# Optimization experiments

Measured on AMD Instinct MI355X. Metric: run time of the kernel, lower is better.

## Reference

```python
import jax, jax.numpy as jnp
import numpy as np

B, T, C, V, L, H, HS = 64, 256, 256, 65, 6, 8, 32


def _ln(x, g, b, eps=1e-5):
    mu = jnp.mean(x, axis=-1, keepdims=True)
    var = jnp.mean(jnp.square(x - mu), axis=-1, keepdims=True)
    return (x - mu) * jax.lax.rsqrt(var + eps) * g + b


def setup_inputs() -> dict:
    key = jax.random.key(0)
    ks = jax.random.split(key, 28)
    n = lambda k, s: jax.random.normal(k, s, dtype=jnp.float32) * 0.02
    return {
        "idx": jax.random.randint(ks[0], (B, T), 0, V),
        "targets": jax.random.randint(ks[1], (B, T), 0, V),
        "tok_emb": n(ks[2], (V, C)),
        "pos_emb": n(ks[3], (T, C)),
        "wq": n(ks[4], (L, H, C, HS)), "bq": n(ks[5], (L, H, HS)),
        "wk": n(ks[6], (L, H, C, HS)), "bk": n(ks[7], (L, H, HS)),
        "wv": n(ks[8], (L, H, C, HS)), "bv": n(ks[9], (L, H, HS)),
        "wo": n(ks[10], (L, C, C)), "bo": n(ks[11], (L, C)),
        "ln1_g": jnp.ones((L, C), jnp.float32), "ln1_b": jnp.zeros((L, C), jnp.float32),
        "w1": n(ks[12], (L, C, 4 * C)), "b1": n(ks[13], (L, 4 * C)),
        "w2": n(ks[14], (L, 4 * C, C)), "b2": n(ks[15], (L, C)),
        "ln2_g": jnp.ones((L, C), jnp.float32), "ln2_b": jnp.zeros((L, C), jnp.float32),
        "lnf_g": jnp.ones((C,), jnp.float32), "lnf_b": jnp.zeros((C,), jnp.float32),
        "lm_w": n(ks[16], (C, V)), "lm_b": n(ks[17], (V,)),
    }


def reference(idx, targets, tok_emb, pos_emb, wq, bq, wk, bk, wv, bv, wo, bo,
              ln1_g, ln1_b, w1, b1, w2, b2, ln2_g, ln2_b, lnf_g, lnf_b, lm_w, lm_b):
    Bc, Tc = idx.shape
    x = tok_emb[idx] + pos_emb[:Tc]  # [B,T,C]
    causal = jnp.tril(jnp.ones((Tc, Tc), dtype=bool))
    scale = C ** (-0.5)  # NOTE: original scales by n_embd**-0.5, not head_size
    for l in range(L):
        xn = _ln(x, ln1_g[l], ln1_b[l])
        q = jnp.einsum('btc,hcd->bhtd', xn, wq[l]) + bq[l][None, :, None, :]
        k = jnp.einsum('btc,hcd->bhtd', xn, wk[l]) + bk[l][None, :, None, :]
        v = jnp.einsum('btc,hcd->bhtd', xn, wv[l]) + bv[l][None, :, None, :]
        s = jnp.einsum('bhtd,bhsd->bhts', q, k) * scale
        s = jnp.where(causal, s, -jnp.inf)
        a = jax.nn.softmax(s, axis=-1)  # dropout is identity in eval
        o = jnp.einsum('bhts,bhsd->bhtd', a, v)
        o = o.transpose(0, 2, 1, 3).reshape(Bc, Tc, C)  # concat heads
        x = x + o @ wo[l] + bo[l]
        xn2 = _ln(x, ln2_g[l], ln2_b[l])
        h = jax.nn.relu(xn2 @ w1[l] + b1[l])
        x = x + h @ w2[l] + b2[l]
    x = _ln(x, lnf_g, lnf_b)
    logits = (x @ lm_w + lm_b).reshape(Bc * Tc, V)
    logp = jax.nn.log_softmax(logits, axis=-1)
    tgt = targets.reshape(-1)
    loss = -jnp.mean(logp[jnp.arange(Bc * Tc), tgt])
    return logits, loss
```

## Files before the change

### kernel.cpp

```cpp
#include <hip/hip_runtime.h>
#include <hip/hip_bf16.h>
#include <math.h>

#define BB 64
#define TT 256
#define CC 256
#define VV 65
#define LL 6
#define HH 8
#define BT (BB*TT)

typedef unsigned short u16;
typedef __attribute__((ext_vector_type(8))) _Float16 h8v;
typedef __attribute__((ext_vector_type(4))) float f4v;
typedef __attribute__((ext_vector_type(4))) unsigned short u16x4;

typedef const unsigned int __attribute__((address_space(1))) gu32;
typedef unsigned int       __attribute__((address_space(3))) lu32;

__device__ inline u16 f2h(float f) { _Float16 h = (_Float16)f; return *(u16*)&h; }

__device__ inline void gld_lds16(const void* g, void* l) {
    __builtin_amdgcn_global_load_lds((gu32*)g, (lu32*)l, 16, 0, 0);
}


__device__ inline void pack_dev(const float* __restrict__ src, u16* __restrict__ dst,
                                int K, int N, int NT, int KT, int id) {
    int perLayer = NT * KT * 8192;
    int l = id / perLayer; int rem = id - l * perLayer;
    int tile = rem >> 13, within = rem & 8191;
    int nT = tile / KT, kT = tile - nT * KT;
    int colIn = within >> 6, u = within & 63;
    int s = (u >> 3) ^ (colIn & 7);
    int k = kT * 64 + s * 8 + (u & 7);
    int n = nT * 128 + colIn;
    float v = (n < N) ? src[((size_t)l * K + k) * N + n] : 0.f;
    dst[((size_t)l * NT * KT + tile) * 8192 + within] = f2h(v);
}

#define E_QKV (LL*24*8192)
#define E_WO  (LL*8*8192)
#define E_W1  (LL*32*8192)
#define E_W2  (LL*32*8192)
#define E_LM  (4*8192)
#define E_QB  (LL*768)
#define E_TOT (E_QKV+E_WO+E_W1+E_W2+E_LM+E_QB)

__global__ __launch_bounds__(256)
void pack_all(const float* __restrict__ wq, const float* __restrict__ wk,
              const float* __restrict__ wv, const float* __restrict__ wo,
              const float* __restrict__ w1, const float* __restrict__ w2,
              const float* __restrict__ lmw,
              const float* __restrict__ bq, const float* __restrict__ bk,
              const float* __restrict__ bv,
              u16* __restrict__ qkvT, u16* __restrict__ woT, u16* __restrict__ w1T,
              u16* __restrict__ w2T, u16* __restrict__ lmT, float* __restrict__ Bp) {
    int id = blockIdx.x * 256 + threadIdx.x;
    if (id < E_QKV) {
        const int perLayer = 24 * 8192;
        int l = id / perLayer; int rem = id - l * perLayer;
        int tile = rem >> 13, within = rem & 8191;
        int nT = tile >> 2, kT = tile & 3;
        int colIn = within >> 6, u = within & 63;
        int s = (u >> 3) ^ (colIn & 7);
        int k = kT * 64 + s * 8 + (u & 7);
        int n = nT * 128 + colIn;
        int which = n >> 8, hd = n & 255, h = hd >> 5, d = hd & 31;
        const float* src = (which == 0) ? wq : (which == 1) ? wk : wv;
        float v = src[(((size_t)l * HH + h) * CC + k) * 32 + d];
        qkvT[((size_t)l * 24 + tile) * 8192 + within] = f2h(v);
        return;
    }
    id -= E_QKV;
    if (id < E_WO) { pack_dev(wo, woT, 256, 256, 2, 4, id); return; }
    id -= E_WO;
    if (id < E_W1) { pack_dev(w1, w1T, 256, 1024, 8, 4, id); return; }
    id -= E_W1;
    if (id < E_W2) { pack_dev(w2, w2T, 1024, 256, 2, 16, id); return; }
    id -= E_W2;
    if (id < E_LM) { pack_dev(lmw, lmT, 256, VV, 1, 4, id); return; }
    id -= E_LM;
    if (id < E_QB) {
        int l = id / 768, j = id % 768;
        int which = j >> 8, hd = j & 255, h = hd >> 5, d = hd & 31;
        const float* src = (which == 0) ? bq : (which == 1) ? bk : bv;
        Bp[id] = src[((size_t)l * HH + h) * 32 + d];
    }
}

__global__ __launch_bounds__(256)
void embed_kernel(const int* __restrict__ idx, const float* __restrict__ te,
                  const float* __restrict__ pe, float* __restrict__ x) {
    int i = blockIdx.x * blockDim.x + threadIdx.x;
    if (i >= BT * 64) return;
    int bt = i >> 6, c4 = i & 63;
    int tok = idx[bt];
    int t = bt & (TT - 1);
    float4 a = ((const float4*)te)[(size_t)tok * 64 + c4];
    float4 p = ((const float4*)pe)[(size_t)t * 64 + c4];
    float4 o; o.x = a.x + p.x; o.y = a.y + p.y; o.z = a.z + p.z; o.w = a.w + p.w;
    ((float4*)x)[i] = o;
}

__global__ __launch_bounds__(256)
void ln_kernel(const float* __restrict__ x, const float* __restrict__ g,
               const float* __restrict__ b, u16* __restrict__ outT) {
    int lane = threadIdx.x & 63;
    int wave = threadIdx.x >> 6;
    int row = blockIdx.x * 4 + wave;
    float4 v = ((const float4*)(x + (size_t)row * CC))[lane];
    float s = v.x + v.y + v.z + v.w;
    #pragma unroll
    for (int m = 1; m < 64; m <<= 1) s += __shfl_xor(s, m, 64);
    float mu = s * (1.f / CC);
    float dx = v.x - mu, dy = v.y - mu, dz = v.z - mu, dw = v.w - mu;
    float vs = dx * dx + dy * dy + dz * dz + dw * dw;
    #pragma unroll
    for (int m = 1; m < 64; m <<= 1) vs += __shfl_xor(vs, m, 64);
    float rs = rsqrtf(vs * (1.f / CC) + 1e-5f);
    float4 gv = ((const float4*)g)[lane];
    float4 bv = ((const float4*)b)[lane];
    float o[4];
    o[0] = dx * rs * gv.x + bv.x;
    o[1] = dy * rs * gv.y + bv.y;
    o[2] = dz * rs * gv.z + bv.z;
    o[3] = dw * rs * gv.w + bv.w;
    int rIn = row & 127, mT = row >> 7;
    int kT = lane >> 4;
    int kIn = (lane * 4) & 63;
    int slot = kIn >> 3, j = kIn & 7;
    size_t base = ((size_t)mT * 4 + kT) * 8192;
    int ub = rIn * 64 + ((slot ^ (rIn & 7)) << 3) + j;
    u16x4 hv;
    #pragma unroll
    for (int q = 0; q < 4; ++q) hv[q] = f2h(o[q]);
    *(u16x4*)(outT + base + ub) = hv;
}

template<int EPI>
__global__ __launch_bounds__(512, 4)
void gemm_mfma(const u16* __restrict__ At, const u16* __restrict__ Bt,
               const float* __restrict__ bias, float* __restrict__ Co,
               u16* __restrict__ CoT, int KTfull, int KTc, int NT, int N, int KTout) {
    __shared__ __align__(16) char lds[65536];
    int tid = threadIdx.x;
    int l = tid & 63, w = tid >> 6;
    int nwg = gridDim.x;
    int id = blockIdx.x;
    int cpx = nwg >> 3;
    id = (id & 7) * cpx + (id >> 3);
    int mT = id / NT, nT = id - mT * NT;
    int ktBase = blockIdx.y * KTc;

    const char* Abase = (const char*)(At + ((size_t)mT * KTfull + ktBase) * 8192);
    const char* Bbase = (const char*)(Bt + ((size_t)nT * KTfull + ktBase) * 8192);
    int wm = w >> 1, wn = w & 1;

    f4v acc[2][4];
    #pragma unroll
    for (int i = 0; i < 2; ++i)
        #pragma unroll
        for (int j = 0; j < 4; ++j) acc[i][j] = (f4v)0.f;

    int lrow = l & 15, lg = l >> 4;

    #define STAGE(buf, kt) {                                           \
        char* la = lds + (buf) * 32768 + w * 2048;                     \
        char* lb = lds + (buf) * 32768 + 16384 + w * 2048;             \
        const char* ga = Abase + (kt) * 16384 + w * 2048 + l * 16;     \
        const char* gb = Bbase + (kt) * 16384 + w * 2048 + l * 16;     \
        _Pragma("unroll")                                              \
        for (int j = 0; j < 2; ++j) {                                  \
            gld_lds16(ga + j * 1024, la + j * 1024);                   \
            gld_lds16(gb + j * 1024, lb + j * 1024);                   \
        } }

    STAGE(0, 0);
    __syncthreads();
    int cur = 0;
    for (int kt = 0; kt < KTc; ++kt) {
        if (kt + 1 < KTc) STAGE(cur ^ 1, kt + 1);
        const char* lb0 = lds + cur * 32768;
        #pragma unroll
        for (int kh = 0; kh < 2; ++kh) {
            h8v ah[2], bh[4];
            #pragma unroll
            for (int mi = 0; mi < 2; ++mi) {
                int rc = wm * 32 + mi * 16 + lrow;
                ah[mi] = *(const h8v*)(lb0 + rc * 128 + 16 * ((kh * 4 + lg) ^ (rc & 7)));
            }
            #pragma unroll
            for (int ni = 0; ni < 4; ++ni) {
                int rc = wn * 64 + ni * 16 + lrow;
                bh[ni] = *(const h8v*)(lb0 + 16384 + rc * 128 + 16 * ((kh * 4 + lg) ^ (rc & 7)));
            }
            #pragma unroll
            for (int mi = 0; mi < 2; ++mi)
                #pragma unroll
                for (int ni = 0; ni < 4; ++ni)
                    acc[mi][ni] = __builtin_amdgcn_mfma_f32_16x16x32_f16(ah[mi], bh[ni], acc[mi][ni], 0, 0, 0);
        }
        __syncthreads();
        cur ^= 1;
    }
    #undef STAGE

    int colbase = nT * 128 + wn * 64;
    if (EPI == 0) {
        #pragma unroll
        for (int mi = 0; mi < 2; ++mi) {
            int r0 = mT * 128 + wm * 32 + mi * 16 + lg * 4;
            #pragma unroll
            for (int ni = 0; ni < 4; ++ni) {
                int cg = colbase + ni * 16 + lrow;
                float bv = bias[cg];
                #pragma unroll
                for (int q = 0; q < 4; ++q)
                    CoT[(size_t)(r0 + q) * N + cg] = f2h(acc[mi][ni][q] + bv);
            }
        }
    } else if (EPI == 2) {
        #pragma unroll
        for (int mi = 0; mi < 2; ++mi) {
            int r0 = mT * 128 + wm * 32 + mi * 16 + lg * 4;
            #pragma unroll
            for (int ni = 0; ni < 4; ++ni) {
                int cg = colbase + ni * 16 + lrow;
                float bv = bias[cg];
                int kTo = cg >> 6, kIn = cg & 63;
                size_t tbase = ((size_t)mT * KTout + kTo) * 8192;
                #pragma unroll
                for (int q = 0; q < 4; ++q) {
                    int rIn = (r0 + q) & 127;
                    float f = fmaxf(acc[mi][ni][q] + bv, 0.f);
                    int ub = rIn * 64 + (((kIn >> 3) ^ (rIn & 7)) << 3) + (kIn & 7);
                    CoT[tbase + ub] = f2h(f);
                }
            }
        }
    } else if (EPI == 3) {
        #pragma unroll
        for (int mi = 0; mi < 2; ++mi) {
            int r0 = mT * 128 + wm * 32 + mi * 16 + lg * 4;
            #pragma unroll
            for (int ni = 0; ni < 4; ++ni) {
                int cg = colbase + ni * 16 + lrow;
                if (cg < VV) {
                    float bv = bias[cg];
                    #pragma unroll
                    for (int q = 0; q < 4; ++q)
                        Co[(size_t)(r0 + q) * VV + cg] = acc[mi][ni][q] + bv;
                }
            }
        }
    } else {
        #pragma unroll
        for (int mi = 0; mi < 2; ++mi) {
            int r0 = mT * 128 + wm * 32 + mi * 16 + lg * 4;
            #pragma unroll
            for (int ni = 0; ni < 4; ++ni) {
                int cg = colbase + ni * 16 + lrow;
                float bv = (ktBase == 0) ? bias[cg] : 0.f;
                #pragma unroll
                for (int q = 0; q < 4; ++q)
                    atomicAdd(Co + (size_t)(r0 + q) * N + cg, acc[mi][ni][q] + bv);
            }
        }
    }
}

__global__ __launch_bounds__(256)
void attn_mfma(const u16* __restrict__ qkv, u16* __restrict__ outT) {
    __shared__ __align__(16) char lds[42496];
    int bh = blockIdx.x;
    bh = (bh & 7) * 64 + (bh >> 3);
    int b = bh >> 3, h = bh & 7;
    const u16* base = qkv + (size_t)b * TT * 768;
    int tid = threadIdx.x;
    int w = tid >> 6, l = tid & 63;
    int li = l & 15, g = l >> 4;

    {
        int r0 = tid >> 3, c = tid & 7;
        #pragma unroll
        for (int it = 0; it < 8; ++it) {
            int t = it * 32 + r0;
            u16x4 kv = *(const u16x4*)(base + (size_t)t * 768 + 256 + h * 32 + c * 4);
            u16x4 vv = *(const u16x4*)(base + (size_t)t * 768 + 512 + h * 32 + c * 4);
            *(u16x4*)(lds + t * 80 + c * 8) = kv;
            *(u16*)(lds + 20480 + (c * 4 + 0) * 528 + t * 2) = vv[0];
            *(u16*)(lds + 20480 + (c * 4 + 1) * 528 + t * 2) = vv[1];
            *(u16*)(lds + 20480 + (c * 4 + 2) * 528 + t * 2) = vv[2];
            *(u16*)(lds + 20480 + (c * 4 + 3) * 528 + t * 2) = vv[3];
        }
    }
    __syncthreads();

    char* Pb = lds + 37376 + w * 1280;
    int mts[4] = {w, 7 - w, 8 + w, 15 - w};
    #pragma unroll
    for (int im = 0; im < 4; ++im) {
        int mt = mts[im];
        int mq = mt * 16;
        h8v aq = *(const h8v*)(base + (size_t)(mq + li) * 768 + h * 32 + g * 8);

        f4v o0 = (f4v)0.f, o1 = (f4v)0.f;
        float mrun0 = -1e30f, mrun1 = -1e30f, mrun2 = -1e30f, mrun3 = -1e30f;
        float lrun0 = 0.f, lrun1 = 0.f, lrun2 = 0.f, lrun3 = 0.f;
        int nu = (mt >> 1) + 1;
        for (int kt = 0; kt < nu; ++kt) {
            int kb = kt * 32;
            h8v kf0 = *(const h8v*)(lds + (kb + li) * 80 + g * 16);
            h8v kf1 = *(const h8v*)(lds + (kb + 16 + li) * 80 + g * 16);
            f4v s0 = __builtin_amdgcn_mfma_f32_16x16x32_f16(aq, kf0, (f4v)0.f, 0, 0, 0);
            f4v s1 = __builtin_amdgcn_mfma_f32_16x16x32_f16(aq, kf1, (f4v)0.f, 0, 0, 0);
            bool maskunit = (kt == nu - 1);
            float p0[4], p1[4];
            float* mr[4] = {&mrun0, &mrun1, &mrun2, &mrun3};
            float* lr[4] = {&lrun0, &lrun1, &lrun2, &lrun3};
            #pragma unroll
            for (int qq = 0; qq < 4; ++qq) {
                float v0 = s0[qq] * 0.0625f;
                float v1 = s1[qq] * 0.0625f;
                if (maskunit) {
                    int qg = mq + g * 4 + qq;
                    if (kb + li > qg)      v0 = -1e30f;
                    if (kb + 16 + li > qg) v1 = -1e30f;
                }
                float tm = fmaxf(v0, v1);
                #pragma unroll
                for (int msk = 1; msk < 16; msk <<= 1)
                    tm = fmaxf(tm, __shfl_xor(tm, msk, 64));
                float mold = *mr[qq];
                float mnew = fmaxf(mold, tm);
                float corr = __expf(mold - mnew);
                float e0 = __expf(v0 - mnew);
                float e1 = __expf(v1 - mnew);
                float ts = e0 + e1;
                #pragma unroll
                for (int msk = 1; msk < 16; msk <<= 1)
                    ts += __shfl_xor(ts, msk, 64);
                *lr[qq] = *lr[qq] * corr + ts;
                *mr[qq] = mnew;
                o0[qq] *= corr; o1[qq] *= corr;
                p0[qq] = e0; p1[qq] = e1;
            }
            #pragma unroll
            for (int qq = 0; qq < 4; ++qq) {
                *(u16*)(Pb + (g * 4 + qq) * 80 + li * 2)        = f2h(p0[qq]);
                *(u16*)(Pb + (g * 4 + qq) * 80 + (16 + li) * 2) = f2h(p1[qq]);
            }
            h8v pf  = *(const h8v*)(Pb + li * 80 + g * 16);
            h8v vf0 = *(const h8v*)(lds + 20480 + li * 528        + kb * 2 + g * 16);
            h8v vf1 = *(const h8v*)(lds + 20480 + (16 + li) * 528 + kb * 2 + g * 16);
            o0 = __builtin_amdgcn_mfma_f32_16x16x32_f16(pf, vf0, o0, 0, 0, 0);
            o1 = __builtin_amdgcn_mfma_f32_16x16x32_f16(pf, vf1, o1, 0, 0, 0);
        }
        float invs[4] = {1.f / lrun0, 1.f / lrun1, 1.f / lrun2, 1.f / lrun3};
        #pragma unroll
        for (int qq = 0; qq < 4; ++qq) {
            int tok = mq + g * 4 + qq;
            int rIn = tok & 127;
            size_t tb = ((size_t)(b * 2 + (tok >> 7)) * 4 + (h >> 1)) * 8192;
            float f0 = o0[qq] * invs[qq];
            float f1 = o1[qq] * invs[qq];
            int kIn0 = (h & 1) * 32 + li;
            int kIn1 = kIn0 + 16;
            int ub0 = rIn * 64 + (((kIn0 >> 3) ^ (rIn & 7)) << 3) + (kIn0 & 7);
            int ub1 = rIn * 64 + (((kIn1 >> 3) ^ (rIn & 7)) << 3) + (kIn1 & 7);
            outT[tb + ub0] = f2h(f0);
            outT[tb + ub1] = f2h(f1);
        }
    }
}

__global__ __launch_bounds__(256)
void loss_kernel(const float* __restrict__ lg, const int* __restrict__ tgt,
                 float* __restrict__ loss) {
    int row = blockIdx.x * 256 + threadIdx.x;
    const float* r = lg + (size_t)row * VV;
    float mx = -INFINITY;
    for (int v = 0; v < VV; ++v) mx = fmaxf(mx, r[v]);
    float se = 0.f;
    for (int v = 0; v < VV; ++v) se += __expf(r[v] - mx);
    float nl = mx + __logf(se) - r[tgt[row]];
    #pragma unroll
    for (int m = 1; m < 64; m <<= 1) nl += __shfl_xor(nl, m, 64);
    __shared__ float wsum[4];
    int lane = threadIdx.x & 63, wv = threadIdx.x >> 6;
    if (lane == 0) wsum[wv] = nl;
    __syncthreads();
    if (threadIdx.x == 0)
        atomicAdd(loss, (wsum[0] + wsum[1] + wsum[2] + wsum[3]) * (1.f / BT));
}

extern "C" void kernel_launch(void* const* d_in, const int* in_sizes, int n_in,
                              void* d_out, int out_size, void* d_ws, size_t ws_size,
                              hipStream_t stream) {
    const int*   idx  = (const int*)d_in[0];
    const int*   tgt  = (const int*)d_in[1];
    const float* te   = (const float*)d_in[2];
    const float* pe   = (const float*)d_in[3];
    const float* wq   = (const float*)d_in[4];
    const float* bq   = (const float*)d_in[5];
    const float* wk   = (const float*)d_in[6];
    const float* bk   = (const float*)d_in[7];
    const float* wv   = (const float*)d_in[8];
    const float* bv   = (const float*)d_in[9];
    const float* wo   = (const float*)d_in[10];
    const float* bo   = (const float*)d_in[11];
    const float* ln1g = (const float*)d_in[12];
    const float* ln1b = (const float*)d_in[13];
    const float* w1   = (const float*)d_in[14];
    const float* b1   = (const float*)d_in[15];
    const float* w2   = (const float*)d_in[16];
    const float* b2   = (const float*)d_in[17];
    const float* ln2g = (const float*)d_in[18];
    const float* ln2b = (const float*)d_in[19];
    const float* lnfg = (const float*)d_in[20];
    const float* lnfb = (const float*)d_in[21];
    const float* lmw  = (const float*)d_in[22];
    const float* lmb  = (const float*)d_in[23];
    float* out = (float*)d_out;

    char* base = (char*)d_ws;
    float* x       = (float*)(base);
    u16*   qkvh    = (u16*)  (base + (16ll << 20));
    u16*   hiddenT = (u16*)  (base + (40ll << 20));
    u16*   xnT     = (u16*)  (base + (72ll << 20));
    u16*   qkvT    = (u16*)  (base + (80ll << 20));
    u16*   woT     = (u16*)  (base + (83ll << 20));
    u16*   w1T     = (u16*)  (base + (84ll << 20));
    u16*   w2T     = (u16*)  (base + (87ll << 20));
    u16*   lmT     = (u16*)  (base + (90ll << 20));
    float* Bp      = (float*)(base + (91ll << 20));

    pack_all<<<dim3(E_TOT / 256), 256, 0, stream>>>(wq, wk, wv, wo, w1, w2, lmw,
                                                    bq, bk, bv,
                                                    qkvT, woT, w1T, w2T, lmT, Bp);
    embed_kernel<<<dim3((BT * 64) / 256), 256, 0, stream>>>(idx, te, pe, x);

    for (int l = 0; l < LL; ++l) {
        ln_kernel<<<dim3(BT / 4), 256, 0, stream>>>(x, ln1g + l * CC, ln1b + l * CC, xnT);
        gemm_mfma<0><<<dim3(128 * 6, 1), 512, 0, stream>>>(
            xnT, qkvT + (size_t)l * 196608, Bp + l * 768, nullptr, qkvh, 4, 4, 6, 768, 0);
        attn_mfma<<<dim3(BB * HH), 256, 0, stream>>>(qkvh, xnT);
        gemm_mfma<4><<<dim3(128 * 2, 2), 512, 0, stream>>>(
            xnT, woT + (size_t)l * 65536, bo + l * CC, x, nullptr, 4, 2, 2, 256, 0);
        ln_kernel<<<dim3(BT / 4), 256, 0, stream>>>(x, ln2g + l * CC, ln2b + l * CC, xnT);
        gemm_mfma<2><<<dim3(128 * 8, 1), 512, 0, stream>>>(
            xnT, w1T + (size_t)l * 262144, b1 + l * 1024, nullptr, hiddenT, 4, 4, 8, 1024, 16);
        gemm_mfma<4><<<dim3(128 * 2, 2), 512, 0, stream>>>(
            hiddenT, w2T + (size_t)l * 262144, b2 + l * CC, x, nullptr, 16, 8, 2, 256, 0);
    }
    ln_kernel<<<dim3(BT / 4), 256, 0, stream>>>(x, lnfg, lnfb, xnT);
    gemm_mfma<3><<<dim3(128 * 1, 1), 512, 0, stream>>>(
        xnT, lmT, lmb, out, nullptr, 4, 4, 1, VV, 0);

    hipMemsetAsync(out + (size_t)BT * VV, 0, sizeof(float), stream);
    loss_kernel<<<dim3(BT / 256), 256, 0, stream>>>(out, tgt, out + (size_t)BT * VV);
}
```

Before: 980.4 us.

## Fuse all stages into one cooperative persistent megakernel with grid syncs

Replaces the sequence of about 45 separate kernel launches (pack, embed, layernorm, GEMMs, attention, loss) with one cooperative kernel of 256 persistent blocks. Stages are separated by grid.sync() and work is spread with grid-stride loops over tiles. This removes per-launch overhead and inter-kernel gaps. In exchange it runs at most 256 blocks at 2 per CU, and adds grid-wide barrier cost at every stage boundary.

Measured after the change: 2.362 ms. +141.0%, slower.

```diff
diff --git a/kernel.cpp b/kernel.cpp
--- a/kernel.cpp
+++ b/kernel.cpp
@@ -1,6 +1,9 @@
 #include <hip/hip_runtime.h>
 #include <hip/hip_bf16.h>
+#include <hip/hip_cooperative_groups.h>
 #include <math.h>
+
+namespace cg = cooperative_groups;
 
 #define BB 64
 #define TT 256
@@ -25,8 +28,24 @@
 }
 
 
-__device__ inline void pack_dev(const float* __restrict__ src, u16* __restrict__ dst,
-                                int K, int N, int NT, int KT, int id) {
+#define E_QKV (LL*24*8192)
+#define E_WO  (LL*8*8192)
+#define E_W1  (LL*32*8192)
+#define E_W2  (LL*32*8192)
+#define E_LM  (4*8192)
+#define E_QB  (LL*768)
+#define E_TOT (E_QKV+E_WO+E_W1+E_W2+E_LM+E_QB)
+
+struct MegaArgs {
+    const int *idx, *tgt;
+    const float *te, *pe, *wq, *bq, *wk, *bk, *wv, *bv, *wo, *bo;
+    const float *ln1g, *ln1b, *w1, *b1, *w2, *b2, *ln2g, *ln2b, *lnfg, *lnfb, *lmw, *lmb;
+    float* out;
+    float* x; u16 *qkvh, *hiddenT, *xnT, *qkvT, *woT, *w1T, *w2T, *lmT; float* Bp;
+};
+
+__device__ void pack_dev(const float* __restrict__ src, u16* __restrict__ dst,
+                         int K, int N, int NT, int KT, int id) {
     int perLayer = NT * KT * 8192;
     int l = id / perLayer; int rem = id - l * perLayer;
     int tile = rem >> 13, within = rem & 8191;
@@ -39,24 +58,7 @@
     dst[((size_t)l * NT * KT + tile) * 8192 + within] = f2h(v);
 }
 
-#define E_QKV (LL*24*8192)
-#define E_WO  (LL*8*8192)
-#define E_W1  (LL*32*8192)
-#define E_W2  (LL*32*8192)
-#define E_LM  (4*8192)
-#define E_QB  (LL*768)
-#define E_TOT (E_QKV+E_WO+E_W1+E_W2+E_LM+E_QB)
-
-__global__ __launch_bounds__(256)
-void pack_all(const float* __restrict__ wq, const float* __restrict__ wk,
-              const float* __restrict__ wv, const float* __restrict__ wo,
-              const float* __restrict__ w1, const float* __restrict__ w2,
-              const float* __restrict__ lmw,
-              const float* __restrict__ bq, const float* __restrict__ bk,
-              const float* __restrict__ bv,
-              u16* __restrict__ qkvT, u16* __restrict__ woT, u16* __restrict__ w1T,
-              u16* __restrict__ w2T, u16* __restrict__ lmT, float* __restrict__ Bp) {
-    int id = blockIdx.x * 256 + threadIdx.x;
+__device__ void pack_one(int id, const MegaArgs& a) {
     if (id < E_QKV) {
         const int perLayer = 24 * 8192;
         int l = id / perLayer; int rem = id - l * perLayer;
@@ -67,103 +69,71 @@
         int k = kT * 64 + s * 8 + (u & 7);
         int n = nT * 128 + colIn;
         int which = n >> 8, hd = n & 255, h = hd >> 5, d = hd & 31;
-        const float* src = (which == 0) ? wq : (which == 1) ? wk : wv;
+        const float* src = (which == 0) ? a.wq : (which == 1) ? a.wk : a.wv;
         float v = src[(((size_t)l * HH + h) * CC + k) * 32 + d];
-        qkvT[((size_t)l * 24 + tile) * 8192 + within] = f2h(v);
+        a.qkvT[((size_t)l * 24 + tile) * 8192 + within] = f2h(v);
         return;
     }
     id -= E_QKV;
-    if (id < E_WO) { pack_dev(wo, woT, 256, 256, 2, 4, id); return; }
+    if (id < E_WO) { pack_dev(a.wo, a.woT, 256, 256, 2, 4, id); return; }
     id -= E_WO;
-    if (id < E_W1) { pack_dev(w1, w1T, 256, 1024, 8, 4, id); return; }
+    if (id < E_W1) { pack_dev(a.w1, a.w1T, 256, 1024, 8, 4, id); return; }
     id -= E_W1;
-    if (id < E_W2) { pack_dev(w2, w2T, 1024, 256, 2, 16, id); return; }
+    if (id < E_W2) { pack_dev(a.w2, a.w2T, 1024, 256, 2, 16, id); return; }
     id -= E_W2;
-    if (id < E_LM) { pack_dev(lmw, lmT, 256, VV, 1, 4, id); return; }
+    if (id < E_LM) { pack_dev(a.lmw, a.lmT, 256, VV, 1, 4, id); return; }
     id -= E_LM;
     if (id < E_QB) {
         int l = id / 768, j = id % 768;
         int which = j >> 8, hd = j & 255, h = hd >> 5, d = hd & 31;
-        const float* src = (which == 0) ? bq : (which == 1) ? bk : bv;
-        Bp[id] = src[((size_t)l * HH + h) * 32 + d];
-    }
-}
-
-__global__ __launch_bounds__(256)
-void embed_kernel(const int* __restrict__ idx, const float* __restrict__ te,
-                  const float* __restrict__ pe, float* __restrict__ x) {
-    int i = blockIdx.x * blockDim.x + threadIdx.x;
-    if (i >= BT * 64) return;
-    int bt = i >> 6, c4 = i & 63;
-    int tok = idx[bt];
-    int t = bt & (TT - 1);
-    float4 a = ((const float4*)te)[(size_t)tok * 64 + c4];
-    float4 p = ((const float4*)pe)[(size_t)t * 64 + c4];
-    float4 o; o.x = a.x + p.x; o.y = a.y + p.y; o.z = a.z + p.z; o.w = a.w + p.w;
-    ((float4*)x)[i] = o;
-}
-
-__global__ __launch_bounds__(256)
-void ln_kernel(const float* __restrict__ x, const float* __restrict__ g,
-               const float* __restrict__ b, u16* __restrict__ outT) {
-    int lane = threadIdx.x & 63;
-    int wave = threadIdx.x >> 6;
-    int row = blockIdx.x * 4 + wave;
-    float4 v = ((const float4*)(x + (size_t)row * CC))[lane];
-    float s = v.x + v.y + v.z + v.w;
-    #pragma unroll
-    for (int m = 1; m < 64; m <<= 1) s += __shfl_xor(s, m, 64);
-    float mu = s * (1.f / CC);
-    float dx = v.x - mu, dy = v.y - mu, dz = v.z - mu, dw = v.w - mu;
-    float vs = dx * dx + dy * dy + dz * dz + dw * dw;
-    #pragma unroll
-    for (int m = 1; m < 64; m <<= 1) vs += __shfl_xor(vs, m, 64);
-    float rs = rsqrtf(vs * (1.f / CC) + 1e-5f);
+        const float* src = (which == 0) ? a.bq : (which == 1) ? a.bk : a.bv;
+        a.Bp[id] = src[((size_t)l * HH + h) * 32 + d];
+    }
+}
+
+__device__ void ln_stage(const float* __restrict__ x, const float* __restrict__ g,
+                         const float* __restrict__ b, u16* __restrict__ outT,
+                         int tid, int bid) {
+    int lane = tid & 63;
+    int gwave = bid * 8 + (tid >> 6);
     float4 gv = ((const float4*)g)[lane];
     float4 bv = ((const float4*)b)[lane];
-    float o[4];
-    o[0] = dx * rs * gv.x + bv.x;
-    o[1] = dy * rs * gv.y + bv.y;
-    o[2] = dz * rs * gv.z + bv.z;
-    o[3] = dw * rs * gv.w + bv.w;
-    int rIn = row & 127, mT = row >> 7;
     int kT = lane >> 4;
     int kIn = (lane * 4) & 63;
     int slot = kIn >> 3, j = kIn & 7;
-    size_t base = ((size_t)mT * 4 + kT) * 8192;
-    int ub = rIn * 64 + ((slot ^ (rIn & 7)) << 3) + j;
-    u16x4 hv;
     #pragma unroll
-    for (int q = 0; q < 4; ++q) hv[q] = f2h(o[q]);
-    *(u16x4*)(outT + base + ub) = hv;
+    for (int i = 0; i < 8; ++i) {
+        int row = i * 2048 + gwave;
+        float4 v = ((const float4*)(x + (size_t)row * CC))[lane];
+        float s = v.x + v.y + v.z + v.w;
+        #pragma unroll
+        for (int m = 1; m < 64; m <<= 1) s += __shfl_xor(s, m, 64);
+        float mu = s * (1.f / CC);
+        float dx = v.x - mu, dy = v.y - mu, dz = v.z - mu, dw = v.w - mu;
+        float vs = dx * dx + dy * dy + dz * dz + dw * dw;
+        #pragma unroll
+        for (int m = 1; m < 64; m <<= 1) vs += __shfl_xor(vs, m, 64);
+        float rs = rsqrtf(vs * (1.f / CC) + 1e-5f);
+        int rIn = row & 127, mT = row >> 7;
+        size_t base = ((size_t)mT * 4 + kT) * 8192;
+        int ub = rIn * 64 + ((slot ^ (rIn & 7)) << 3) + j;
+        u16x4 hv;
+        hv[0] = f2h(dx * rs * gv.x + bv.x);
+        hv[1] = f2h(dy * rs * gv.y + bv.y);
+        hv[2] = f2h(dz * rs * gv.z + bv.z);
+        hv[3] = f2h(dw * rs * gv.w + bv.w);
+        *(u16x4*)(outT + base + ub) = hv;
+    }
 }
 
 template<int EPI>
-__global__ __launch_bounds__(512, 4)
-void gemm_mfma(const u16* __restrict__ At, const u16* __restrict__ Bt,
-               const float* __restrict__ bias, float* __restrict__ Co,
-               u16* __restrict__ CoT, int KTfull, int KTc, int NT, int N, int KTout) {
-    __shared__ __align__(16) char lds[65536];
-    int tid = threadIdx.x;
+__device__ void gemm_stage(char* lds, const u16* __restrict__ At, const u16* __restrict__ Bt,
+                           const float* __restrict__ bias, float* __restrict__ Co,
+                           u16* __restrict__ CoT, int KTfull, int KTc, int NUNITS,
+                           int NT, int N, int KTout, int tid, int bid) {
     int l = tid & 63, w = tid >> 6;
-    int nwg = gridDim.x;
-    int id = blockIdx.x;
-    int cpx = nwg >> 3;
-    id = (id & 7) * cpx + (id >> 3);
-    int mT = id / NT, nT = id - mT * NT;
-    int ktBase = blockIdx.y * KTc;
-
-    const char* Abase = (const char*)(At + ((size_t)mT * KTfull + ktBase) * 8192);
-    const char* Bbase = (const char*)(Bt + ((size_t)nT * KTfull + ktBase) * 8192);
+    int lrow = l & 15, lg = l >> 4;
     int wm = w >> 1, wn = w & 1;
-
-    f4v acc[2][4];
-    #pragma unroll
-    for (int i = 0; i < 2; ++i)
-        #pragma unroll
-        for (int j = 0; j < 4; ++j) acc[i][j] = (f4v)0.f;
-
-    int lrow = l & 15, lg = l >> 4;
 
     #define STAGE(buf, kt) {                                           \
         char* la = lds + (buf) * 32768 + w * 2048;                     \
@@ -171,293 +141,330 @@
         const char* ga = Abase + (kt) * 16384 + w * 2048 + l * 16;     \
         const char* gb = Bbase + (kt) * 16384 + w * 2048 + l * 16;     \
         _Pragma("unroll")                                              \
-        for (int j = 0; j < 2; ++j) {                                  \
-            gld_lds16(ga + j * 1024, la + j * 1024);                   \
-            gld_lds16(gb + j * 1024, lb + j * 1024);                   \
+        for (int jj = 0; jj < 2; ++jj) {                               \
+            gld_lds16(ga + jj * 1024, la + jj * 1024);                 \
+            gld_lds16(gb + jj * 1024, lb + jj * 1024);                 \
         } }
 
-    STAGE(0, 0);
-    __syncthreads();
-    int cur = 0;
-    for (int kt = 0; kt < KTc; ++kt) {
-        if (kt + 1 < KTc) STAGE(cur ^ 1, kt + 1);
-        const char* lb0 = lds + cur * 32768;
+    for (int u = bid; u < NUNITS; u += 256) {
+        int tileId = u, ktBase = 0;
+        if (EPI == 4) {
+            int ntile = NUNITS >> 1;
+            if (u >= ntile) { tileId = u - ntile; ktBase = KTc; }
+        }
+        int mT = tileId / NT, nT = tileId - mT * NT;
+        const char* Abase = (const char*)(At + ((size_t)mT * KTfull + ktBase) * 8192);
+        const char* Bbase = (const char*)(Bt + ((size_t)nT * KTfull + ktBase) * 8192);
+
+        f4v acc[2][4];
         #pragma unroll
-        for (int kh = 0; kh < 2; ++kh) {
-            h8v ah[2], bh[4];
+        for (int i = 0; i < 2; ++i)
+            #pragma unroll
+            for (int j = 0; j < 4; ++j) acc[i][j] = (f4v)0.f;
+
+        STAGE(0, 0);
+        __syncthreads();
+        int cur = 0;
+        for (int kt = 0; kt < KTc; ++kt) {
+            if (kt + 1 < KTc) STAGE(cur ^ 1, kt + 1);
+            const char* lb0 = lds + cur * 32768;
+            #pragma unroll
+            for (int kh = 0; kh < 2; ++kh) {
+                h8v ah[2], bh[4];
+                #pragma unroll
+                for (int mi = 0; mi < 2; ++mi) {
+                    int rc = wm * 32 + mi * 16 + lrow;
+                    ah[mi] = *(const h8v*)(lb0 + rc * 128 + 16 * ((kh * 4 + lg) ^ (rc & 7)));
+                }
+                #pragma unroll
+                for (int ni = 0; ni < 4; ++ni) {
+                    int rc = wn * 64 + ni * 16 + lrow;
+                    bh[ni] = *(const h8v*)(lb0 + 16384 + rc * 128 + 16 * ((kh * 4 + lg) ^ (rc & 7)));
+                }
+                #pragma unroll
+                for (int mi = 0; mi < 2; ++mi)
+                    #pragma unroll
+                    for (int ni = 0; ni < 4; ++ni)
+                        acc[mi][ni] = __builtin_amdgcn_mfma_f32_16x16x32_f16(ah[mi], bh[ni], acc[mi][ni], 0, 0, 0);
+            }
+            __syncthreads();
+            cur ^= 1;
+        }
+
+        int colbase = nT * 128 + wn * 64;
+        if (EPI == 0) {
             #pragma unroll
             for (int mi = 0; mi < 2; ++mi) {
-                int rc = wm * 32 + mi * 16 + lrow;
-                ah[mi] = *(const h8v*)(lb0 + rc * 128 + 16 * ((kh * 4 + lg) ^ (rc & 7)));
-            }
-            #pragma unroll
-            for (int ni = 0; ni < 4; ++ni) {
-                int rc = wn * 64 + ni * 16 + lrow;
-                bh[ni] = *(const h8v*)(lb0 + 16384 + rc * 128 + 16 * ((kh * 4 + lg) ^ (rc & 7)));
-            }
-            #pragma unroll
-            for (int mi = 0; mi < 2; ++mi)
-                #pragma unroll
-                for (int ni = 0; ni < 4; ++ni)
-                    acc[mi][ni] = __builtin_amdgcn_mfma_f32_16x16x32_f16(ah[mi], bh[ni], acc[mi][ni], 0, 0, 0);
+                int r0 = mT * 128 + wm * 32 + mi * 16 + lg * 4;
+                #pragma unroll
+                for (int ni = 0; ni < 4; ++ni) {
+                    int cg = colbase + ni * 16 + lrow;
+                    float bv = bias[cg];
+                    #pragma unroll
+                    for (int q = 0; q < 4; ++q)
+                        CoT[(size_t)(r0 + q) * N + cg] = f2h(acc[mi][ni][q] + bv);
+                }
+            }
+        } else if (EPI == 2) {
+            #pragma unroll
+            for (int mi = 0; mi < 2; ++mi) {
+                int r0 = mT * 128 + wm * 32 + mi * 16 + lg * 4;
+                #pragma unroll
+                for (int ni = 0; ni < 4; ++ni) {
+                    int cg = colbase + ni * 16 + lrow;
+                    float bv = bias[cg];
+                    int kTo = cg >> 6, kIn = cg & 63;
+                    size_t tbase = ((size_t)mT * KTout + kTo) * 8192;
+                    #pragma unroll
+                    for (int q = 0; q < 4; ++q) {
+                        int rIn = (r0 + q) & 127;
+                        float f = fmaxf(acc[mi][ni][q] + bv, 0.f);
+                        int ub = rIn * 64 + (((kIn >> 3) ^ (rIn & 7)) << 3) + (kIn & 7);
+                        CoT[tbase + ub] = f2h(f);
+                    }
+                }
+            }
+        } else if (EPI == 3) {
+            #pragma unroll
+            for (int mi = 0; mi < 2; ++mi) {
+                int r0 = mT * 128 + wm * 32 + mi * 16 + lg * 4;
+                #pragma unroll
+                for (int ni = 0; ni < 4; ++ni) {
+                    int cg = colbase + ni * 16 + lrow;
+                    if (cg < VV) {
+                        float bv = bias[cg];
+                        #pragma unroll
+                        for (int q = 0; q < 4; ++q)
+                            Co[(size_t)(r0 + q) * VV + cg] = acc[mi][ni][q] + bv;
+                    }
+                }
+            }
+        } else {
+            #pragma unroll
+            for (int mi = 0; mi < 2; ++mi) {
+                int r0 = mT * 128 + wm * 32 + mi * 16 + lg * 4;
+                #pragma unroll
+                for (int ni = 0; ni < 4; ++ni) {
+                    int cg = colbase + ni * 16 + lrow;
+                    float bv = (ktBase == 0) ? bias[cg] : 0.f;
+                    #pragma unroll
+                    for (int q = 0; q < 4; ++q)
+                        atomicAdd(Co + (size_t)(r0 + q) * N + cg, acc[mi][ni][q] + bv);
+                }
+            }
+        }
+    }
+    #undef STAGE
+}
+
+__device__ void attn_stage(char* lds, const u16* __restrict__ qkv,
+                           u16* __restrict__ outT, int tid, int bid) {
+    int w = tid >> 6, l = tid & 63;
+    int li = l & 15, g = l >> 4;
+    for (int u = bid; u < 512; u += 256) {
+        int bb = u >> 3, h = u & 7;
+        const u16* base = qkv + (size_t)bb * TT * 768;
+        __syncthreads();
+        {
+            int r0 = tid >> 3, c = tid & 7;
+            #pragma unroll
+            for (int it = 0; it < 4; ++it) {
+                int t = it * 64 + r0;
+                u16x4 kv = *(const u16x4*)(base + (size_t)t * 768 + 256 + h * 32 + c * 4);
+                u16x4 vv = *(const u16x4*)(base + (size_t)t * 768 + 512 + h * 32 + c * 4);
+                *(u16x4*)(lds + t * 80 + c * 8) = kv;
+                *(u16*)(lds + 20480 + (c * 4 + 0) * 528 + t * 2) = vv[0];
+                *(u16*)(lds + 20480 + (c * 4 + 1) * 528 + t * 2) = vv[1];
+                *(u16*)(lds + 20480 + (c * 4 + 2) * 528 + t * 2) = vv[2];
+                *(u16*)(lds + 20480 + (c * 4 + 3) * 528 + t * 2) = vv[3];
+            }
         }
         __syncthreads();
-        cur ^= 1;
-    }
-    #undef STAGE
-
-    int colbase = nT * 128 + wn * 64;
-    if (EPI == 0) {
+
+        char* Pb = lds + 37376 + w * 1280;
+        int mts[2] = {w, 15 - w};
         #pragma unroll
-        for (int mi = 0; mi < 2; ++mi) {
-            int r0 = mT * 128 + wm * 32 + mi * 16 + lg * 4;
-            #pragma unroll
-            for (int ni = 0; ni < 4; ++ni) {
-                int cg = colbase + ni * 16 + lrow;
-                float bv = bias[cg];
-                #pragma unroll
-                for (int q = 0; q < 4; ++q)
-                    CoT[(size_t)(r0 + q) * N + cg] = f2h(acc[mi][ni][q] + bv);
+        for (int im = 0; im < 2; ++im) {
+            int mt = mts[im];
+            int mq = mt * 16;
+            h8v aq = *(const h8v*)(base + (size_t)(mq + li) * 768 + h * 32 + g * 8);
+
+            f4v o0 = (f4v)0.f, o1 = (f4v)0.f;
+            float mrun0 = -1e30f, mrun1 = -1e30f, mrun2 = -1e30f, mrun3 = -1e30f;
+            float lrun0 = 0.f, lrun1 = 0.f, lrun2 = 0.f, lrun3 = 0.f;
+            int nu = (mt >> 1) + 1;
+            for (int kt = 0; kt < nu; ++kt) {
+                int kb = kt * 32;
+                h8v kf0 = *(const h8v*)(lds + (kb + li) * 80 + g * 16);
+                h8v kf1 = *(const h8v*)(lds + (kb + 16 + li) * 80 + g * 16);
+                f4v s0 = __builtin_amdgcn_mfma_f32_16x16x32_f16(aq, kf0, (f4v)0.f, 0, 0, 0);
+                f4v s1 = __builtin_amdgcn_mfma_f32_16x16x32_f16(aq, kf1, (f4v)0.f, 0, 0, 0);
+                bool maskunit = (kt == nu - 1);
+                float p0[4], p1[4];
+                float* mr[4] = {&mrun0, &mrun1, &mrun2, &mrun3};
+                float* lr[4] = {&lrun0, &lrun1, &lrun2, &lrun3};
+                #pragma unroll
+                for (int qq = 0; qq < 4; ++qq) {
+                    float v0 = s0[qq] * 0.0625f;
+                    float v1 = s1[qq] * 0.0625f;
+                    if (maskunit) {
+                        int qg = mq + g * 4 + qq;
+                        if (kb + li > qg)      v0 = -1e30f;
+                        if (kb + 16 + li > qg) v1 = -1e30f;
+                    }
+                    float tm = fmaxf(v0, v1);
+                    #pragma unroll
+                    for (int msk = 1; msk < 16; msk <<= 1)
+                        tm = fmaxf(tm, __shfl_xor(tm, msk, 64));
+                    float mold = *mr[qq];
+                    float mnew = fmaxf(mold, tm);
+                    float corr = __expf(mold - mnew);
+                    float e0 = __expf(v0 - mnew);
+                    float e1 = __expf(v1 - mnew);
+                    float ts = e0 + e1;
+                    #pragma unroll
+                    for (int msk = 1; msk < 16; msk <<= 1)
+                        ts += __shfl_xor(ts, msk, 64);
+                    *lr[qq] = *lr[qq] * corr + ts;
+                    *mr[qq] = mnew;
+                    o0[qq] *= corr; o1[qq] *= corr;
+                    p0[qq] = e0; p1[qq] = e1;
+                }
+                #pragma unroll
+                for (int qq = 0; qq < 4; ++qq) {
+                    *(u16*)(Pb + (g * 4 + qq) * 80 + li * 2)        = f2h(p0[qq]);
+                    *(u16*)(Pb + (g * 4 + qq) * 80 + (16 + li) * 2) = f2h(p1[qq]);
+                }
+                h8v pf  = *(const h8v*)(Pb + li * 80 + g * 16);
+                h8v vf0 = *(const h8v*)(lds + 20480 + li * 528        + kb * 2 + g * 16);
+                h8v vf1 = *(const h8v*)(lds + 20480 + (16 + li) * 528 + kb * 2 + g * 16);
+                o0 = __builtin_amdgcn_mfma_f32_16x16x32_f16(pf, vf0, o0, 0, 0, 0);
+                o1 = __builtin_amdgcn_mfma_f32_16x16x32_f16(pf, vf1, o1, 0, 0, 0);
+            }
+            float invs[4] = {1.f / lrun0, 1.f / lrun1, 1.f / lrun2, 1.f / lrun3};
+            #pragma unroll
+            for (int qq = 0; qq < 4; ++qq) {
+                int tok = mq + g * 4 + qq;
+                int rIn = tok & 127;
+                size_t tb = ((size_t)(bb * 2 + (tok >> 7)) * 4 + (h >> 1)) * 8192;
+                float f0 = o0[qq] * invs[qq];
+                float f1 = o1[qq] * invs[qq];
+                int kIn0 = (h & 1) * 32 + li;
+                int kIn1 = kIn0 + 16;
+                int ub0 = rIn * 64 + (((kIn0 >> 3) ^ (rIn & 7)) << 3) + (kIn0 & 7);
+                int ub1 = rIn * 64 + (((kIn1 >> 3) ^ (rIn & 7)) << 3) + (kIn1 & 7);
+                outT[tb + ub0] = f2h(f0);
+                outT[tb + ub1] = f2h(f1);
             }
         }
-    } else if (EPI == 2) {
-        #pragma unroll
-        for (int mi = 0; mi < 2; ++mi) {
-            int r0 = mT * 128 + wm * 32 + mi * 16 + lg * 4;
-            #pragma unroll
-            for (int ni = 0; ni < 4; ++ni) {
-                int cg = colbase + ni * 16 + lrow;
-                float bv = bias[cg];
-                int kTo = cg >> 6, kIn = cg & 63;
-                size_t tbase = ((size_t)mT * KTout + kTo) * 8192;
-                #pragma unroll
-                for (int q = 0; q < 4; ++q) {
-                    int rIn = (r0 + q) & 127;
-                    float f = fmaxf(acc[mi][ni][q] + bv, 0.f);
-                    int ub = rIn * 64 + (((kIn >> 3) ^ (rIn & 7)) << 3) + (kIn & 7);
-                    CoT[tbase + ub] = f2h(f);
-                }
-            }
-        }
-    } else if (EPI == 3) {
-        #pragma unroll
-        for (int mi = 0; mi < 2; ++mi) {
-            int r0 = mT * 128 + wm * 32 + mi * 16 + lg * 4;
-            #pragma unroll
-            for (int ni = 0; ni < 4; ++ni) {
-                int cg = colbase + ni * 16 + lrow;
-                if (cg < VV) {
-                    float bv = bias[cg];
-                    #pragma unroll
-                    for (int q = 0; q < 4; ++q)
-                        Co[(size_t)(r0 + q) * VV + cg] = acc[mi][ni][q] + bv;
-                }
-            }
-        }
-    } else {
-        #pragma unroll
-        for (int mi = 0; mi < 2; ++mi) {
-            int r0 = mT * 128 + wm * 32 + mi * 16 + lg * 4;
-            #pragma unroll
-            for (int ni = 0; ni < 4; ++ni) {
-                int cg = colbase + ni * 16 + lrow;
-                float bv = (ktBase == 0) ? bias[cg] : 0.f;
-                #pragma unroll
-                for (int q = 0; q < 4; ++q)
-                    atomicAdd(Co + (size_t)(r0 + q) * N + cg, acc[mi][ni][q] + bv);
-            }
-        }
-    }
-}
-
-__global__ __launch_bounds__(256)
-void attn_mfma(const u16* __restrict__ qkv, u16* __restrict__ outT) {
-    __shared__ __align__(16) char lds[42496];
-    int bh = blockIdx.x;
-    bh = (bh & 7) * 64 + (bh >> 3);
-    int b = bh >> 3, h = bh & 7;
-    const u16* base = qkv + (size_t)b * TT * 768;
-    int tid = threadIdx.x;
-    int w = tid >> 6, l = tid & 63;
-    int li = l & 15, g = l >> 4;
-
-    {
-        int r0 = tid >> 3, c = tid & 7;
-        #pragma unroll
-        for (int it = 0; it < 8; ++it) {
-            int t = it * 32 + r0;
-            u16x4 kv = *(const u16x4*)(base + (size_t)t * 768 + 256 + h * 32 + c * 4);
-            u16x4 vv = *(const u16x4*)(base + (size_t)t * 768 + 512 + h * 32 + c * 4);
-            *(u16x4*)(lds + t * 80 + c * 8) = kv;
-            *(u16*)(lds + 20480 + (c * 4 + 0) * 528 + t * 2) = vv[0];
-            *(u16*)(lds + 20480 + (c * 4 + 1) * 528 + t * 2) = vv[1];
-            *(u16*)(lds + 20480 + (c * 4 + 2) * 528 + t * 2) = vv[2];
-            *(u16*)(lds + 20480 + (c * 4 + 3) * 528 + t * 2) = vv[3];
-        }
-    }
-    __syncthreads();
-
-    char* Pb = lds + 37376 + w * 1280;
-    int mts[4] = {w, 7 - w, 8 + w, 15 - w};
-    #pragma unroll
-    for (int im = 0; im < 4; ++im) {
-        int mt = mts[im];
-        int mq = mt * 16;
-        h8v aq = *(const h8v*)(base + (size_t)(mq + li) * 768 + h * 32 + g * 8);
-
-        f4v o0 = (f4v)0.f, o1 = (f4v)0.f;
-        float mrun0 = -1e30f, mrun1 = -1e30f, mrun2 = -1e30f, mrun3 = -1e30f;
-        float lrun0 = 0.f, lrun1 = 0.f, lrun2 = 0.f, lrun3 = 0.f;
-        int nu = (mt >> 1) + 1;
-        for (int kt = 0; kt < nu; ++kt) {
-            int kb = kt * 32;
-            h8v kf0 = *(const h8v*)(lds + (kb + li) * 80 + g * 16);
-            h8v kf1 = *(const h8v*)(lds + (kb + 16 + li) * 80 + g * 16);
-            f4v s0 = __builtin_amdgcn_mfma_f32_16x16x32_f16(aq, kf0, (f4v)0.f, 0, 0, 0);
-            f4v s1 = __builtin_amdgcn_mfma_f32_16x16x32_f16(aq, kf1, (f4v)0.f, 0, 0, 0);
-            bool maskunit = (kt == nu - 1);
-            float p0[4], p1[4];
-            float* mr[4] = {&mrun0, &mrun1, &mrun2, &mrun3};
-            float* lr[4] = {&lrun0, &lrun1, &lrun2, &lrun3};
-            #pragma unroll
-            for (int qq = 0; qq < 4; ++qq) {
-                float v0 = s0[qq] * 0.0625f;
-                float v1 = s1[qq] * 0.0625f;
-                if (maskunit) {
-                    int qg = mq + g * 4 + qq;
-                    if (kb + li > qg)      v0 = -1e30f;
-                    if (kb + 16 + li > qg) v1 = -1e30f;
-                }
-                float tm = fmaxf(v0, v1);
-                #pragma unroll
-                for (int msk = 1; msk < 16; msk <<= 1)
-                    tm = fmaxf(tm, __shfl_xor(tm, msk, 64));
-                float mold = *mr[qq];
-                float mnew = fmaxf(mold, tm);
-                float corr = __expf(mold - mnew);
-                float e0 = __expf(v0 - mnew);
-                float e1 = __expf(v1 - mnew);
-                float ts = e0 + e1;
-                #pragma unroll
-                for (int msk = 1; msk < 16; msk <<= 1)
-                    ts += __shfl_xor(ts, msk, 64);
-                *lr[qq] = *lr[qq] * corr + ts;
-                *mr[qq] = mnew;
-                o0[qq] *= corr; o1[qq] *= corr;
-                p0[qq] = e0; p1[qq] = e1;
-            }
-            #pragma unroll
-            for (int qq = 0; qq < 4; ++qq) {
-                *(u16*)(Pb + (g * 4 + qq) * 80 + li * 2)        = f2h(p0[qq]);
-                *(u16*)(Pb + (g * 4 + qq) * 80 + (16 + li) * 2) = f2h(p1[qq]);
-            }
-            h8v pf  = *(const h8v*)(Pb + li * 80 + g * 16);
-            h8v vf0 = *(const h8v*)(lds + 20480 + li * 528        + kb * 2 + g * 16);
-            h8v vf1 = *(const h8v*)(lds + 20480 + (16 + li) * 528 + kb * 2 + g * 16);
-            o0 = __builtin_amdgcn_mfma_f32_16x16x32_f16(pf, vf0, o0, 0, 0, 0);
-            o1 = __builtin_amdgcn_mfma_f32_16x16x32_f16(pf, vf1, o1, 0, 0, 0);
-        }
-        float invs[4] = {1.f / lrun0, 1.f / lrun1, 1.f / lrun2, 1.f / lrun3};
-        #pragma unroll
-        for (int qq = 0; qq < 4; ++qq) {
-            int tok = mq + g * 4 + qq;
-            int rIn = tok & 127;
-            size_t tb = ((size_t)(b * 2 + (tok >> 7)) * 4 + (h >> 1)) * 8192;
-            float f0 = o0[qq] * invs[qq];
-            float f1 = o1[qq] * invs[qq];
-            int kIn0 = (h & 1) * 32 + li;
-            int kIn1 = kIn0 + 16;
-            int ub0 = rIn * 64 + (((kIn0 >> 3) ^ (rIn & 7)) << 3) + (kIn0 & 7);
-            int ub1 = rIn * 64 + (((kIn1 >> 3) ^ (rIn & 7)) << 3) + (kIn1 & 7);
-            outT[tb + ub0] = f2h(f0);
-            outT[tb + ub1] = f2h(f1);
-        }
-    }
-}
-
-__global__ __launch_bounds__(256)
-void loss_kernel(const float* __restrict__ lg, const int* __restrict__ tgt,
-                 float* __restrict__ loss) {
-    int row = blockIdx.x * 256 + threadIdx.x;
-    const float* r = lg + (size_t)row * VV;
-    float mx = -INFINITY;
-    for (int v = 0; v < VV; ++v) mx = fmaxf(mx, r[v]);
-    float se = 0.f;
-    for (int v = 0; v < VV; ++v) se += __expf(r[v] - mx);
-    float nl = mx + __logf(se) - r[tgt[row]];
+    }
+}
+
+__device__ void loss_stage(const float* __restrict__ lg, const int* __restrict__ tgt,
+                           float* __restrict__ loss, int gtid) {
+    float nl = 0.f;
+    if (gtid < BT) {
+        const float* r = lg + (size_t)gtid * VV;
+        float mx = -INFINITY;
+        for (int v = 0; v < VV; ++v) mx = fmaxf(mx, r[v]);
+        float se = 0.f;
+        for (int v = 0; v < VV; ++v) se += __expf(r[v] - mx);
+        nl = mx + __logf(se) - r[tgt[gtid]];
+    }
     #pragma unroll
     for (int m = 1; m < 64; m <<= 1) nl += __shfl_xor(nl, m, 64);
-    __shared__ float wsum[4];
-    int lane = threadIdx.x & 63, wv = threadIdx.x >> 6;
-    if (lane == 0) wsum[wv] = nl;
-    __syncthreads();
-    if (threadIdx.x == 0)
-        atomicAdd(loss, (wsum[0] + wsum[1] + wsum[2] + wsum[3]) * (1.f / BT));
+    if ((gtid & 63) == 0 && gtid < BT)
+        atomicAdd(loss, nl * (1.f / BT));
+}
+
+__global__ __launch_bounds__(512, 2)
+void mega(MegaArgs a) {
+    __shared__ __align__(16) char lds[65536];
+    cg::grid_group grid = cg::this_grid();
+    int tid = threadIdx.x, bid = blockIdx.x;
+    int gtid = bid * 512 + tid;
+
+    for (int e = gtid; e < E_TOT; e += 131072) pack_one(e, a);
+    for (int i = gtid; i < BT * 64; i += 131072) {
+        int bt = i >> 6, c4 = i & 63;
+        int tok = a.idx[bt];
+        int t = bt & (TT - 1);
+        float4 av = ((const float4*)a.te)[(size_t)tok * 64 + c4];
+        float4 p = ((const float4*)a.pe)[(size_t)t * 64 + c4];
+        float4 o; o.x = av.x + p.x; o.y = av.y + p.y; o.z = av.z + p.z; o.w = av.w + p.w;
+        ((float4*)a.x)[i] = o;
+    }
+    if (gtid == 0) a.out[(size_t)BT * VV] = 0.f;
+    grid.sync();
+
+    for (int l = 0; l < LL; ++l) {
+        ln_stage(a.x, a.ln1g + l * CC, a.ln1b + l * CC, a.xnT, tid, bid);
+        grid.sync();
+        gemm_stage<0>(lds, a.xnT, a.qkvT + (size_t)l * 196608, a.Bp + l * 768,
+                      nullptr, a.qkvh, 4, 4, 768, 6, 768, 0, tid, bid);
+        grid.sync();
+        attn_stage(lds, a.qkvh, a.xnT, tid, bid);
+        grid.sync();
+        gemm_stage<4>(lds, a.xnT, a.woT + (size_t)l * 65536, a.bo + l * CC,
+                      a.x, nullptr, 4, 2, 512, 2, 256, 0, tid, bid);
+        grid.sync();
+        ln_stage(a.x, a.ln2g + l * CC, a.ln2b + l * CC, a.xnT, tid, bid);
+        grid.sync();
+        gemm_stage<2>(lds, a.xnT, a.w1T + (size_t)l * 262144, a.b1 + l * 1024,
+                      nullptr, a.hiddenT, 4, 4, 1024, 8, 1024, 16, tid, bid);
+        grid.sync();
+        gemm_stage<4>(lds, a.hiddenT, a.w2T + (size_t)l * 262144, a.b2 + l * CC,
+                      a.x, nullptr, 16, 8, 512, 2, 256, 0, tid, bid);
+        grid.sync();
+    }
+    ln_stage(a.x, a.lnfg, a.lnfb, a.xnT, tid, bid);
+    grid.sync();
+    gemm_stage<3>(lds, a.xnT, a.lmT, a.lmb, a.out, nullptr, 4, 4, 128, 1, VV, 0, tid, bid);
+    grid.sync();
+    loss_stage(a.out, a.tgt, a.out + (size_t)BT * VV, gtid);
 }
 
 extern "C" void kernel_launch(void* const* d_in, const int* in_sizes, int n_in,
                               void* d_out, int out_size, void* d_ws, size_t ws_size,
                               hipStream_t stream) {
-    const int*   idx  = (const int*)d_in[0];
-    const int*   tgt  = (const int*)d_in[1];
-    const float* te   = (const float*)d_in[2];
-    const float* pe   = (const float*)d_in[3];
-    const float* wq   = (const float*)d_in[4];
-    const float* bq   = (const float*)d_in[5];
-    const float* wk   = (const float*)d_in[6];
-    const float* bk   = (const float*)d_in[7];
-    const float* wv   = (const float*)d_in[8];
-    const float* bv   = (const float*)d_in[9];
-    const float* wo   = (const float*)d_in[10];
-    const float* bo   = (const float*)d_in[11];
-    const float* ln1g = (const float*)d_in[12];
-    const float* ln1b = (const float*)d_in[13];
-    const float* w1   = (const float*)d_in[14];
-    const float* b1   = (const float*)d_in[15];
-    const float* w2   = (const float*)d_in[16];
-    const float* b2   = (const float*)d_in[17];
-    const float* ln2g = (const float*)d_in[18];
-    const float* ln2b = (const float*)d_in[19];
-    const float* lnfg = (const float*)d_in[20];
-    const float* lnfb = (const float*)d_in[21];
-    const float* lmw  = (const float*)d_in[22];
-    const float* lmb  = (const float*)d_in[23];
-    float* out = (float*)d_out;
-
     char* base = (char*)d_ws;
-    float* x       = (float*)(base);
-    u16*   qkvh    = (u16*)  (base + (16ll << 20));
-    u16*   hiddenT = (u16*)  (base + (40ll << 20));
-    u16*   xnT     = (u16*)  (base + (72ll << 20));
-    u16*   qkvT    = (u16*)  (base + (80ll << 20));
-    u16*   woT     = (u16*)  (base + (83ll << 20));
-    u16*   w1T     = (u16*)  (base + (84ll << 20));
-    u16*   w2T     = (u16*)  (base + (87ll << 20));
-    u16*   lmT     = (u16*)  (base + (90ll << 20));
-    float* Bp      = (float*)(base + (91ll << 20));
-
-    pack_all<<<dim3(E_TOT / 256), 256, 0, stream>>>(wq, wk, wv, wo, w1, w2, lmw,
-                                                    bq, bk, bv,
-                                                    qkvT, woT, w1T, w2T, lmT, Bp);
-    embed_kernel<<<dim3((BT * 64) / 256), 256, 0, stream>>>(idx, te, pe, x);
-
-    for (int l = 0; l < LL; ++l) {
-        ln_kernel<<<dim3(BT / 4), 256, 0, stream>>>(x, ln1g + l * CC, ln1b + l * CC, xnT);
-        gemm_mfma<0><<<dim3(128 * 6, 1), 512, 0, stream>>>(
-            xnT, qkvT + (size_t)l * 196608, Bp + l * 768, nullptr, qkvh, 4, 4, 6, 768, 0);
-        attn_mfma<<<dim3(BB * HH), 256, 0, stream>>>(qkvh, xnT);
-        gemm_mfma<4><<<dim3(128 * 2, 2), 512, 0, stream>>>(
-            xnT, woT + (size_t)l * 65536, bo + l * CC, x, nullptr, 4, 2, 2, 256, 0);
-        ln_kernel<<<dim3(BT / 4), 256, 0, stream>>>(x, ln2g + l * CC, ln2b + l * CC, xnT);
-        gemm_mfma<2><<<dim3(128 * 8, 1), 512, 0, stream>>>(
-            xnT, w1T + (size_t)l * 262144, b1 + l * 1024, nullptr, hiddenT, 4, 4, 8, 1024, 16);
-        gemm_mfma<4><<<dim3(128 * 2, 2), 512, 0, stream>>>(
-            hiddenT, w2T + (size_t)l * 262144, b2 + l * CC, x, nullptr, 16, 8, 2, 256, 0);
-    }
-    ln_kernel<<<dim3(BT / 4), 256, 0, stream>>>(x, lnfg, lnfb, xnT);
-    gemm_mfma<3><<<dim3(128 * 1, 1), 512, 0, stream>>>(
-        xnT, lmT, lmb, out, nullptr, 4, 4, 1, VV, 0);
-
-    hipMemsetAsync(out + (size_t)BT * VV, 0, sizeof(float), stream);
-    loss_kernel<<<dim3(BT / 256), 256, 0, stream>>>(out, tgt, out + (size_t)BT * VV);
-}
+    MegaArgs a;
+    a.idx  = (const int*)d_in[0];
+    a.tgt  = (const int*)d_in[1];
+    a.te   = (const float*)d_in[2];
+    a.pe   = (const float*)d_in[3];
+    a.wq   = (const float*)d_in[4];
+    a.bq   = (const float*)d_in[5];
+    a.wk   = (const float*)d_in[6];
+    a.bk   = (const float*)d_in[7];
+    a.wv   = (const float*)d_in[8];
+    a.bv   = (const float*)d_in[9];
+    a.wo   = (const float*)d_in[10];
+    a.bo   = (const float*)d_in[11];
+    a.ln1g = (const float*)d_in[12];
+    a.ln1b = (const float*)d_in[13];
+    a.w1   = (const float*)d_in[14];
+    a.b1   = (const float*)d_in[15];
+    a.w2   = (const float*)d_in[16];
+    a.b2   = (const float*)d_in[17];
+    a.ln2g = (const float*)d_in[18];
+    a.ln2b = (const float*)d_in[19];
+    a.lnfg = (const float*)d_in[20];
+    a.lnfb = (const float*)d_in[21];
+    a.lmw  = (const float*)d_in[22];
+    a.lmb  = (const float*)d_in[23];
+    a.out  = (float*)d_out;
+    a.x       = (float*)(base);
+    a.qkvh    = (u16*)  (base + (16ll << 20));
+    a.hiddenT = (u16*)  (base + (40ll << 20));
+    a.xnT     = (u16*)  (base + (72ll << 20));
+    a.qkvT    = (u16*)  (base + (80ll << 20));
+    a.woT     = (u16*)  (base + (83ll << 20));
+    a.w1T     = (u16*)  (base + (84ll << 20));
+    a.w2T     = (u16*)  (base + (87ll << 20));
+    a.lmT     = (u16*)  (base + (90ll << 20));
+    a.Bp      = (float*)(base + (91ll << 20));
+
+    void* kargs[] = { (void*)&a };
+    hipLaunchCooperativeKernel(mega, dim3(256), dim3(512), kargs, 0, stream);
+}
```
